# Optimization experiments

Hardware: AMD Instinct MI355X
Metric: run time of the kernel (lower is better)

## Reference

```python
import jax, jax.numpy as jnp
import numpy as np

EMBED = 384
N_HEADS = 6
HEAD_SIZE = EMBED // N_HEADS
B, T = 4, 2048
EPS = 1e-5


def _layernorm(x, g, b):
    mu = jnp.mean(x, axis=-1, keepdims=True)
    var = jnp.mean(jnp.square(x - mu), axis=-1, keepdims=True)
    return (x - mu) * jax.lax.rsqrt(var + EPS) * g + b


def setup_inputs() -> dict:
    key = jax.random.key(0)
    ks = jax.random.split(key, 6)
    s = 0.02
    return {
        "x": jax.random.normal(ks[0], (B, T, EMBED), jnp.float32),
        "Wq": jax.random.normal(ks[1], (N_HEADS, HEAD_SIZE, EMBED), jnp.float32) * s,
        "Wo": jax.random.normal(ks[2], (EMBED, EMBED), jnp.float32) * s,
        "bo": jnp.zeros((EMBED,), jnp.float32),
        "W1": jax.random.normal(ks[3], (EMBED, EMBED), jnp.float32) * s,
        "b1": jnp.zeros((EMBED,), jnp.float32),
        "W2": jax.random.normal(ks[4], (EMBED, EMBED), jnp.float32) * s,
        "b2": jnp.zeros((EMBED,), jnp.float32),
        "g1": jnp.ones((EMBED,), jnp.float32),
        "be1": jnp.zeros((EMBED,), jnp.float32),
        "g2": jnp.ones((EMBED,), jnp.float32),
        "be2": jnp.zeros((EMBED,), jnp.float32),
    }


def reference(x, Wq, Wo, bo, W1, b1, W2, b2, g1, be1, g2, be2):
    # NOTE: original Head uses self.query for q, k AND v (a bug we reproduce):
    # q = k = v = x @ Wq^T per head.
    q = jnp.einsum("bte,hde->bhtd", x, Wq)  # [B,H,T,D]
    scale = HEAD_SIZE ** -0.5
    scores = jnp.einsum("bhtd,bhsd->bhts", q, q) * scale  # [B,H,T,T]
    # torch.tril zeros the upper triangle, then masked_fill(tmp==0, -inf)
    tril = jnp.tril(jnp.ones((T, T), bool))
    scores = jnp.where(tril, scores, 0.0)
    scores = jnp.where(scores == 0.0, -jnp.inf, scores)
    attn = jax.nn.softmax(scores, axis=-1)
    head_out = jnp.einsum("bhts,bhsd->bhtd", attn, q)  # [B,H,T,D]
    cat = head_out.transpose(0, 2, 1, 3).reshape(B, T, EMBED)  # concat heads
    sa = cat @ Wo.T + bo
    x = _layernorm(x + sa, g1, be1)
    ff = jax.nn.relu(x @ W1.T + b1) @ W2.T + b2
    return _layernorm(x + ff, g2, be2)
```

## Files before the change

### kernel.cpp

```cpp
#include <hip/hip_runtime.h>
#include <math.h>

#define BB 4
#define TT 2048
#define EE 384
#define HH 6
#define DD 64
#define MM (BB*TT)

typedef __attribute__((ext_vector_type(8))) short bf16x8;
typedef __attribute__((ext_vector_type(4))) float f32x4;

__device__ __forceinline__ unsigned short f2bf(float f) {
    unsigned int u = __float_as_uint(f);
    u = (u + 0x7FFFu + ((u >> 16) & 1u)) >> 16;
    return (unsigned short)u;
}
__device__ __forceinline__ float bf2f(unsigned short u) {
    return __uint_as_float(((unsigned int)u) << 16);
}
__device__ __forceinline__ unsigned int pk2(float a, float b) {
    return (unsigned int)f2bf(a) | ((unsigned int)f2bf(b) << 16);
}
__device__ __forceinline__ unsigned int cvtpk(float lo, float hi) {
    unsigned int r;
    asm("v_cvt_pk_bf16_f32 %0, %1, %2" : "=v"(r) : "v"(lo), "v"(hi));
    return r;
}

__global__ __launch_bounds__(256) void k_cvt(const float* __restrict__ wq,
                                             const float* __restrict__ wo,
                                             const float* __restrict__ w1,
                                             const float* __restrict__ w2,
                                             unsigned short* __restrict__ wqb,
                                             unsigned short* __restrict__ wob,
                                             unsigned short* __restrict__ w1b,
                                             unsigned short* __restrict__ w2b)
{
    int wi = blockIdx.x / 144, off = (blockIdx.x % 144) * 256;
    const float* s4[4] = {wq, wo, w1, w2};
    unsigned short* d4[4] = {wqb, wob, w1b, w2b};
    const float* src = s4[wi]; unsigned short* dst = d4[wi];
    int i = off + threadIdx.x;
    float4 v = ((const float4*)src)[i];
    uint2 o; o.x = pk2(v.x, v.y); o.y = pk2(v.z, v.w);
    ((uint2*)dst)[i] = o;
}

__global__ __launch_bounds__(256, 2) void k_qgemm(const float* __restrict__ x,
                                                  const unsigned short* __restrict__ W,
                                                  unsigned short* __restrict__ qbf,
                                                  unsigned short* __restrict__ qbfT)
{
    __shared__ unsigned short Xs[32][396];
    __shared__ unsigned short Ts[32][200];
    const int tid = threadIdx.x;
    const int w = tid >> 6, lane = tid & 63;
    const int fr = lane & 15, quad = lane >> 4;
    const int m0 = blockIdx.x * 32;
    const int n0 = blockIdx.y * 192 + w * 48;
    const unsigned short* Wp = W + (size_t)(n0 + fr) * EE + quad * 8;

    {
        const float* xp = x + (size_t)m0 * EE;
        #pragma unroll
        for (int it = 0; it < 12; it++) {
            int idx = it * 1024 + tid * 4;
            int row = idx / EE, col = idx % EE;
            float4 v = *(const float4*)(xp + idx);
            uint2 o; o.x = pk2(v.x, v.y); o.y = pk2(v.z, v.w);
            *(uint2*)&Xs[row][col] = o;
        }
    }

    f32x4 acc[2][3];
    bf16x8 bC[3], bN[3], bT[3];
    #pragma unroll
    for (int mt = 0; mt < 2; mt++)
        #pragma unroll
        for (int nt = 0; nt < 3; nt++) acc[mt][nt] = (f32x4){0.f, 0.f, 0.f, 0.f};
    #pragma unroll
    for (int nt = 0; nt < 3; nt++) bC[nt] = *(const bf16x8*)(Wp + (size_t)nt * 16 * EE);
    #pragma unroll
    for (int nt = 0; nt < 3; nt++) bN[nt] = *(const bf16x8*)(Wp + (size_t)nt * 16 * EE + 32);
    #pragma unroll
    for (int nt = 0; nt < 3; nt++) bT[nt] = bN[nt];
    __syncthreads();

    #pragma unroll
    for (int k0 = 0; k0 < 12; k0++) {
        if (k0 < 10) {
            #pragma unroll
            for (int nt = 0; nt < 3; nt++)
                bT[nt] = *(const bf16x8*)(Wp + (size_t)nt * 16 * EE + (k0 + 2) * 32);
        }
        bf16x8 a0 = *(const bf16x8*)&Xs[fr][k0 * 32 + quad * 8];
        bf16x8 a1 = *(const bf16x8*)&Xs[16 + fr][k0 * 32 + quad * 8];
        #pragma unroll
        for (int nt = 0; nt < 3; nt++) {
            acc[0][nt] = __builtin_amdgcn_mfma_f32_16x16x32_bf16(a0, bC[nt], acc[0][nt], 0, 0, 0);
            acc[1][nt] = __builtin_amdgcn_mfma_f32_16x16x32_bf16(a1, bC[nt], acc[1][nt], 0, 0, 0);
        }
        #pragma unroll
        for (int nt = 0; nt < 3; nt++) { bC[nt] = bN[nt]; bN[nt] = bT[nt]; }
    }

    const int bglob = m0 >> 11, t0 = m0 & 2047;
    #pragma unroll
    for (int nt = 0; nt < 3; nt++) {
        int nl = w * 48 + nt * 16 + fr;
        int n = blockIdx.y * 192 + nl;
        int h = n >> 6, d = n & 63;
        #pragma unroll
        for (int mt = 0; mt < 2; mt++)
            #pragma unroll
            for (int r = 0; r < 4; r++) {
                int ml = mt * 16 + quad * 4 + r;
                unsigned short bf = f2bf(acc[mt][nt][r]);
                qbf[((size_t)(bglob * HH + h) * TT + t0 + ml) * DD + d] = bf;
                Ts[ml][nl] = bf;
            }
    }
    __syncthreads();
    if (tid < 192) {
        int nl = tid;
        int n = blockIdx.y * 192 + nl;
        int h = n >> 6, d = n & 63;
        unsigned short tmp[32];
        #pragma unroll
        for (int i = 0; i < 32; i++) tmp[i] = Ts[i][nl];
        unsigned short* dst = qbfT + ((size_t)(bglob * HH + h) * DD + d) * TT + t0;
        *(uint4*)(dst)      = *(const uint4*)&tmp[0];
        *(uint4*)(dst + 8)  = *(const uint4*)&tmp[8];
        *(uint4*)(dst + 16) = *(const uint4*)&tmp[16];
        *(uint4*)(dst + 24) = *(const uint4*)&tmp[24];
    }
}

__global__ __launch_bounds__(256, 4) void k_attn(const unsigned short* __restrict__ qbf,
                                                 const unsigned short* __restrict__ qbfT,
                                                 unsigned short* __restrict__ cat)
{
    __shared__ unsigned short Ks[2][64][72];
    __shared__ unsigned short Vs[2][64][72];
    __shared__ unsigned short Ps[32][72];
    __shared__ float lsc[32];
    float (*Oc)[68] = (float(*)[68])&Ks[0][0][0];

    const int id = blockIdx.x;
    const int xcd = id & 7, j = id >> 3;
    const int bh = xcd * 3 + (j % 3);
    const int p = j / 3;
    const int bb = bh / HH, hh = bh % HH;
    const int tid = threadIdx.x;
    const int w = tid >> 6, lane = tid & 63;
    const int qhalf = w & 1, keyhalf = w >> 1;
    const int fr = lane & 15, quad = lane >> 4;
    const int fc = quad * 8;
    const unsigned short* qb  = qbf  + (size_t)bh * TT * DD;
    const unsigned short* qtb = qbfT + (size_t)bh * DD * TT;
    const int lr = tid >> 2, lc = (tid & 3) * 16;
    const float EXSC = 0.18033688011112042f;

    #pragma unroll 1
    for (int ph = 0; ph < 2; ph++) {
        const int tile = ph ? (63 - p) : p;
        const int m0 = tile * 32;
        const int nkt = (tile >> 1) + 1;

        uint4 kr0, kr1, vr0, vr1;
        {
            const unsigned short* kp = qb + (size_t)lr * DD + lc;
            kr0 = *(const uint4*)(kp);
            kr1 = *(const uint4*)(kp + 8);
            const unsigned short* vp = qtb + (size_t)lr * TT + lc;
            vr0 = *(const uint4*)(vp);
            vr1 = *(const uint4*)(vp + 8);
        }
        const unsigned short* qp = qb + (size_t)(m0 + qhalf * 16 + fr) * DD + fc;
        const bf16x8 qA0 = *(const bf16x8*)(qp);
        const bf16x8 qA1 = *(const bf16x8*)(qp + 32);

        __syncthreads();
        *(uint4*)&Ks[0][lr][lc]     = kr0;
        *(uint4*)&Ks[0][lr][lc + 8] = kr1;
        *(uint4*)&Vs[0][lr][lc]     = vr0;
        *(uint4*)&Vs[0][lr][lc + 8] = vr1;
        __syncthreads();

        f32x4 accO[4];
        #pragma unroll
        for (int dt = 0; dt < 4; dt++) accO[dt] = (f32x4){0.f, 0.f, 0.f, 0.f};
        float ls[4] = {0.f, 0.f, 0.f, 0.f};
        const int rowbase = m0 + qhalf * 16 + quad * 4;
        const int prow = qhalf * 16 + quad * 4;

        for (int kt = 0; kt < nkt; kt++) {
            const int cur = kt & 1;
            const int s0 = kt * 64;
            if (kt < nkt - 1) {
                const unsigned short* kp = qb + (size_t)(s0 + 64 + lr) * DD + lc;
                kr0 = *(const uint4*)(kp);
                kr1 = *(const uint4*)(kp + 8);
                const unsigned short* vp = qtb + (size_t)lr * TT + s0 + 64 + lc;
                vr0 = *(const uint4*)(vp);
                vr1 = *(const uint4*)(vp + 8);
            }

            f32x4 S[2];
            #pragma unroll
            for (int nt = 0; nt < 2; nt++) {
                f32x4 acc = (f32x4){0.f, 0.f, 0.f, 0.f};
                bf16x8 b0 = *(const bf16x8*)&Ks[cur][keyhalf * 32 + nt * 16 + fr][fc];
                acc = __builtin_amdgcn_mfma_f32_16x16x32_bf16(qA0, b0, acc, 0, 0, 0);
                bf16x8 b1 = *(const bf16x8*)&Ks[cur][keyhalf * 32 + nt * 16 + fr][fc + 32];
                acc = __builtin_amdgcn_mfma_f32_16x16x32_bf16(qA1, b1, acc, 0, 0, 0);
                S[nt] = acc;
            }

            const bool edge = (kt == nkt - 1);
            #pragma unroll
            for (int nt = 0; nt < 2; nt++) {
                const int col = keyhalf * 32 + nt * 16 + fr;
                float pv[4];
                if (edge) {
                    const int jg = s0 + col;
                    #pragma unroll
                    for (int r = 0; r < 4; r++) {
                        float s = S[nt][r];
                        pv[r] = (jg <= rowbase + r && s != 0.0f)
                                ? __builtin_amdgcn_exp2f(s * EXSC) : 0.0f;
                        ls[r] += pv[r];
                    }
                } else {
                    #pragma unroll
                    for (int r = 0; r < 4; r++) {
                        float s = S[nt][r];
                        pv[r] = (s != 0.0f) ? __builtin_amdgcn_exp2f(s * EXSC) : 0.0f;
                        ls[r] += pv[r];
                    }
                }
                unsigned int pk0 = cvtpk(pv[0], pv[1]);
                unsigned int pk1 = cvtpk(pv[2], pv[3]);
                Ps[prow + 0][col] = (unsigned short)(pk0);
                Ps[prow + 1][col] = (unsigned short)(pk0 >> 16);
                Ps[prow + 2][col] = (unsigned short)(pk1);
                Ps[prow + 3][col] = (unsigned short)(pk1 >> 16);
            }

            bf16x8 pA = *(const bf16x8*)&Ps[qhalf * 16 + fr][keyhalf * 32 + fc];
            #pragma unroll
            for (int dt = 0; dt < 4; dt++) {
                bf16x8 v0 = *(const bf16x8*)&Vs[cur][dt * 16 + fr][keyhalf * 32 + fc];
                accO[dt] = __builtin_amdgcn_mfma_f32_16x16x32_bf16(pA, v0, accO[dt], 0, 0, 0);
            }

            if (kt < nkt - 1) {
                *(uint4*)&Ks[cur ^ 1][lr][lc]     = kr0;
                *(uint4*)&Ks[cur ^ 1][lr][lc + 8] = kr1;
                *(uint4*)&Vs[cur ^ 1][lr][lc]     = vr0;
                *(uint4*)&Vs[cur ^ 1][lr][lc + 8] = vr1;
                __syncthreads();
            }
        }

        __syncthreads();
        #pragma unroll
        for (int r = 0; r < 4; r++) {
            #pragma unroll
            for (int o = 1; o < 16; o <<= 1) ls[r] += __shfl_xor(ls[r], o, 64);
        }
        if (keyhalf == 1) {
            #pragma unroll
            for (int dt = 0; dt < 4; dt++)
                #pragma unroll
                for (int r = 0; r < 4; r++)
                    Oc[prow + r][dt * 16 + fr] = accO[dt][r];
            if (fr == 0) {
                #pragma unroll
                for (int r = 0; r < 4; r++) lsc[prow + r] = ls[r];
            }
        }
        __syncthreads();
        if (keyhalf == 0) {
            float il[4];
            #pragma unroll
            for (int r = 0; r < 4; r++) il[r] = 1.0f / (ls[r] + lsc[prow + r]);
            #pragma unroll
            for (int dt = 0; dt < 4; dt++) {
                #pragma unroll
                for (int r = 0; r < 4; r++) {
                    float o = accO[dt][r] + Oc[prow + r][dt * 16 + fr];
                    int t = rowbase + r;
                    cat[((size_t)bb * TT + t) * EE + hh * DD + dt * 16 + fr] =
                        f2bf(o * il[r]);
                }
            }
        }
    }
}

__global__ __launch_bounds__(512, 2) void k_ffn(const unsigned short* __restrict__ catb,
                                                const unsigned short* __restrict__ wob,
                                                const float* __restrict__ bo,
                                                const float* __restrict__ x,
                                                const float* __restrict__ g1,
                                                const float* __restrict__ be1,
                                                const unsigned short* __restrict__ w1b,
                                                const float* __restrict__ b1,
                                                const unsigned short* __restrict__ w2b,
                                                const float* __restrict__ b2,
                                                const float* __restrict__ g2,
                                                const float* __restrict__ be2,
                                                float* __restrict__ out)
{
    __shared__ unsigned short X1s[32][392];
    __shared__ unsigned short H1s[32][392];
    __shared__ float ssum[32][8];
    __shared__ float ssq[32][8];
    const int tid = threadIdx.x;
    const int w = tid >> 6, lane = tid & 63;
    const int fr = lane & 15, quad = lane >> 4;
    const int m0 = blockIdx.x * 32;
    const int n0 = w * 48;

    f32x4 acc[2][3];
    bf16x8 bC[3], bN[3], bT[3];
    const unsigned short* Wp1 = w1b + (size_t)(n0 + fr) * EE + quad * 8;
    const unsigned short* Wp2 = w2b + (size_t)(n0 + fr) * EE + quad * 8;

    {
        const unsigned short* Ap0 = catb + (size_t)(m0 + fr) * EE + quad * 8;
        const unsigned short* Ap1 = Ap0 + 16 * EE;
        const unsigned short* Wp = wob + (size_t)(n0 + fr) * EE + quad * 8;
        #pragma unroll
        for (int mt = 0; mt < 2; mt++)
            #pragma unroll
            for (int nt = 0; nt < 3; nt++) acc[mt][nt] = (f32x4){0.f, 0.f, 0.f, 0.f};
        #pragma unroll
        for (int nt = 0; nt < 3; nt++) bC[nt] = *(const bf16x8*)(Wp + (size_t)nt * 16 * EE);
        #pragma unroll
        for (int nt = 0; nt < 3; nt++) bN[nt] = *(const bf16x8*)(Wp + (size_t)nt * 16 * EE + 32);
        #pragma unroll
        for (int nt = 0; nt < 3; nt++) bT[nt] = bN[nt];
        bf16x8 aC0 = *(const bf16x8*)(Ap0);
        bf16x8 aC1 = *(const bf16x8*)(Ap1);
        bf16x8 aN0 = *(const bf16x8*)(Ap0 + 32);
        bf16x8 aN1 = *(const bf16x8*)(Ap1 + 32);
        bf16x8 aT0 = aN0, aT1 = aN1;
        #pragma unroll
        for (int k0 = 0; k0 < 12; k0++) {
            if (k0 < 10) {
                #pragma unroll
                for (int nt = 0; nt < 3; nt++)
                    bT[nt] = *(const bf16x8*)(Wp + (size_t)nt * 16 * EE + (k0 + 2) * 32);
                aT0 = *(const bf16x8*)(Ap0 + (k0 + 2) * 32);
                aT1 = *(const bf16x8*)(Ap1 + (k0 + 2) * 32);
            }
            #pragma unroll
            for (int nt = 0; nt < 3; nt++) {
                acc[0][nt] = __builtin_amdgcn_mfma_f32_16x16x32_bf16(aC0, bC[nt], acc[0][nt], 0, 0, 0);
                acc[1][nt] = __builtin_amdgcn_mfma_f32_16x16x32_bf16(aC1, bC[nt], acc[1][nt], 0, 0, 0);
            }
            aC0 = aN0; aC1 = aN1; aN0 = aT0; aN1 = aT1;
            #pragma unroll
            for (int nt = 0; nt < 3; nt++) { bC[nt] = bN[nt]; bN[nt] = bT[nt]; }
        }
    }
    #pragma unroll
    for (int nt = 0; nt < 3; nt++) bC[nt] = *(const bf16x8*)(Wp1 + (size_t)nt * 16 * EE);
    #pragma unroll
    for (int nt = 0; nt < 3; nt++) bN[nt] = *(const bf16x8*)(Wp1 + (size_t)nt * 16 * EE + 32);
    {
        float s1[2][4] = {{0.f,0.f,0.f,0.f},{0.f,0.f,0.f,0.f}};
        float s2[2][4] = {{0.f,0.f,0.f,0.f},{0.f,0.f,0.f,0.f}};
        #pragma unroll
        for (int nt = 0; nt < 3; nt++) {
            int n = n0 + nt * 16 + fr;
            float bv = bo[n];
            #pragma unroll
            for (int mt = 0; mt < 2; mt++)
                #pragma unroll
                for (int r = 0; r < 4; r++) {
                    float v = acc[mt][nt][r] + bv
                            + x[(size_t)(m0 + mt * 16 + quad * 4 + r) * EE + n];
                    acc[mt][nt][r] = v;
                    s1[mt][r] += v;
                    s2[mt][r] += v * v;
                }
        }
        #pragma unroll
        for (int mt = 0; mt < 2; mt++)
            #pragma unroll
            for (int r = 0; r < 4; r++) {
                #pragma unroll
                for (int o = 1; o < 16; o <<= 1) {
                    s1[mt][r] += __shfl_xor(s1[mt][r], o, 64);
                    s2[mt][r] += __shfl_xor(s2[mt][r], o, 64);
                }
            }
        if (fr == 0) {
            #pragma unroll
            for (int mt = 0; mt < 2; mt++)
                #pragma unroll
                for (int r = 0; r < 4; r++) {
                    ssum[mt * 16 + quad * 4 + r][w] = s1[mt][r];
                    ssq [mt * 16 + quad * 4 + r][w] = s2[mt][r];
                }
        }
    }
    __syncthreads();
    {
        #pragma unroll
        for (int mt = 0; mt < 2; mt++) {
            float mu[4], rs[4];
            #pragma unroll
            for (int r = 0; r < 4; r++) {
                int row = mt * 16 + quad * 4 + r;
                float t1 = 0.f, t2 = 0.f;
                #pragma unroll
                for (int q = 0; q < 8; q++) { t1 += ssum[row][q]; t2 += ssq[row][q]; }
                mu[r] = t1 * (1.0f / EE);
                float var = t2 * (1.0f / EE) - mu[r] * mu[r];
                rs[r] = rsqrtf(var + 1e-5f);
            }
            #pragma unroll
            for (int nt = 0; nt < 3; nt++) {
                int n = n0 + nt * 16 + fr;
                float gv = g1[n], bev = be1[n];
                #pragma unroll
                for (int r = 0; r < 4; r++) {
                    float v = (acc[mt][nt][r] - mu[r]) * rs[r] * gv + bev;
                    X1s[mt * 16 + quad * 4 + r][n] = f2bf(v);
                }
            }
        }
    }
    __syncthreads();

    {
        #pragma unroll
        for (int mt = 0; mt < 2; mt++)
            #pragma unroll
            for (int nt = 0; nt < 3; nt++) acc[mt][nt] = (f32x4){0.f, 0.f, 0.f, 0.f};
        #pragma unroll
        for (int nt = 0; nt < 3; nt++) bT[nt] = bN[nt];
        #pragma unroll
        for (int k0 = 0; k0 < 12; k0++) {
            if (k0 < 10) {
                #pragma unroll
                for (int nt = 0; nt < 3; nt++)
                    bT[nt] = *(const bf16x8*)(Wp1 + (size_t)nt * 16 * EE + (k0 + 2) * 32);
            }
            bf16x8 a0 = *(const bf16x8*)&X1s[fr][k0 * 32 + quad * 8];
            bf16x8 a1 = *(const bf16x8*)&X1s[16 + fr][k0 * 32 + quad * 8];
            #pragma unroll
            for (int nt = 0; nt < 3; nt++) {
                acc[0][nt] = __builtin_amdgcn_mfma_f32_16x16x32_bf16(a0, bC[nt], acc[0][nt], 0, 0, 0);
                acc[1][nt] = __builtin_amdgcn_mfma_f32_16x16x32_bf16(a1, bC[nt], acc[1][nt], 0, 0, 0);
            }
            #pragma unroll
            for (int nt = 0; nt < 3; nt++) { bC[nt] = bN[nt]; bN[nt] = bT[nt]; }
        }
        #pragma unroll
        for (int nt = 0; nt < 3; nt++) bC[nt] = *(const bf16x8*)(Wp2 + (size_t)nt * 16 * EE);
        #pragma unroll
        for (int nt = 0; nt < 3; nt++) bN[nt] = *(const bf16x8*)(Wp2 + (size_t)nt * 16 * EE + 32);
        #pragma unroll
        for (int nt = 0; nt < 3; nt++) {
            int n = n0 + nt * 16 + fr;
            float bv = b1[n];
            #pragma unroll
            for (int mt = 0; mt < 2; mt++)
                #pragma unroll
                for (int r = 0; r < 4; r++)
                    H1s[mt * 16 + quad * 4 + r][n] = f2bf(fmaxf(acc[mt][nt][r] + bv, 0.0f));
        }
    }
    __syncthreads();

    {
        #pragma unroll
        for (int mt = 0; mt < 2; mt++)
            #pragma unroll
            for (int nt = 0; nt < 3; nt++) acc[mt][nt] = (f32x4){0.f, 0.f, 0.f, 0.f};
        #pragma unroll
        for (int nt = 0; nt < 3; nt++) bT[nt] = bN[nt];
        #pragma unroll
        for (int k0 = 0; k0 < 12; k0++) {
            if (k0 < 10) {
                #pragma unroll
                for (int nt = 0; nt < 3; nt++)
                    bT[nt] = *(const bf16x8*)(Wp2 + (size_t)nt * 16 * EE + (k0 + 2) * 32);
            }
            bf16x8 a0 = *(const bf16x8*)&H1s[fr][k0 * 32 + quad * 8];
            bf16x8 a1 = *(const bf16x8*)&H1s[16 + fr][k0 * 32 + quad * 8];
            #pragma unroll
            for (int nt = 0; nt < 3; nt++) {
                acc[0][nt] = __builtin_amdgcn_mfma_f32_16x16x32_bf16(a0, bC[nt], acc[0][nt], 0, 0, 0);
                acc[1][nt] = __builtin_amdgcn_mfma_f32_16x16x32_bf16(a1, bC[nt], acc[1][nt], 0, 0, 0);
            }
            #pragma unroll
            for (int nt = 0; nt < 3; nt++) { bC[nt] = bN[nt]; bN[nt] = bT[nt]; }
        }
    }
    {
        float s1[2][4] = {{0.f,0.f,0.f,0.f},{0.f,0.f,0.f,0.f}};
        float s2[2][4] = {{0.f,0.f,0.f,0.f},{0.f,0.f,0.f,0.f}};
        #pragma unroll
        for (int nt = 0; nt < 3; nt++) {
            int n = n0 + nt * 16 + fr;
            float bv = b2[n];
            #pragma unroll
            for (int mt = 0; mt < 2; mt++)
                #pragma unroll
                for (int r = 0; r < 4; r++) {
                    float v = acc[mt][nt][r] + bv + bf2f(X1s[mt * 16 + quad * 4 + r][n]);
                    acc[mt][nt][r] = v;
                    s1[mt][r] += v;
                    s2[mt][r] += v * v;
                }
        }
        #pragma unroll
        for (int mt = 0; mt < 2; mt++)
            #pragma unroll
            for (int r = 0; r < 4; r++) {
                #pragma unroll
                for (int o = 1; o < 16; o <<= 1) {
                    s1[mt][r] += __shfl_xor(s1[mt][r], o, 64);
                    s2[mt][r] += __shfl_xor(s2[mt][r], o, 64);
                }
            }
        if (fr == 0) {
            #pragma unroll
            for (int mt = 0; mt < 2; mt++)
                #pragma unroll
                for (int r = 0; r < 4; r++) {
                    ssum[mt * 16 + quad * 4 + r][w] = s1[mt][r];
                    ssq [mt * 16 + quad * 4 + r][w] = s2[mt][r];
                }
        }
    }
    __syncthreads();
    {
        #pragma unroll
        for (int mt = 0; mt < 2; mt++) {
            float mu[4], rs[4];
            #pragma unroll
            for (int r = 0; r < 4; r++) {
                int row = mt * 16 + quad * 4 + r;
                float u1 = 0.f, u2 = 0.f;
                #pragma unroll
                for (int q = 0; q < 8; q++) { u1 += ssum[row][q]; u2 += ssq[row][q]; }
                mu[r] = u1 * (1.0f / EE);
                float var = u2 * (1.0f / EE) - mu[r] * mu[r];
                rs[r] = rsqrtf(var + 1e-5f);
            }
            #pragma unroll
            for (int nt = 0; nt < 3; nt++) {
                int n = n0 + nt * 16 + fr;
                float gv = g2[n], bev = be2[n];
                #pragma unroll
                for (int r = 0; r < 4; r++)
                    out[(size_t)(m0 + mt * 16 + quad * 4 + r) * EE + n] =
                        (acc[mt][nt][r] - mu[r]) * rs[r] * gv + bev;
            }
        }
    }
}

extern "C" void kernel_launch(void* const* d_in, const int* in_sizes, int n_in,
                              void* d_out, int out_size, void* d_ws, size_t ws_size,
                              hipStream_t stream) {
    (void)in_sizes; (void)n_in; (void)out_size; (void)ws_size;
    const float* x   = (const float*)d_in[0];
    const float* Wq  = (const float*)d_in[1];
    const float* Wo  = (const float*)d_in[2];
    const float* bo  = (const float*)d_in[3];
    const float* W1  = (const float*)d_in[4];
    const float* b1  = (const float*)d_in[5];
    const float* W2  = (const float*)d_in[6];
    const float* b2  = (const float*)d_in[7];
    const float* g1  = (const float*)d_in[8];
    const float* be1 = (const float*)d_in[9];
    const float* g2  = (const float*)d_in[10];
    const float* be2 = (const float*)d_in[11];
    float* out = (float*)d_out;

    float* ws = (float*)d_ws;
    const size_t SZ = (size_t)MM * EE;
    float* S1 = ws + SZ;
    float* S2 = ws + 2 * SZ;
    float* S3 = ws + 3 * SZ;

    unsigned short* qbf  = (unsigned short*)S1;
    unsigned short* qbfT = qbf + (size_t)BB * HH * TT * DD;
    unsigned short* catb = (unsigned short*)S2;
    unsigned short* wqb  = (unsigned short*)S3;
    unsigned short* wob  = wqb + (size_t)EE * EE;
    unsigned short* w1b  = wob + (size_t)EE * EE;
    unsigned short* w2b  = w1b + (size_t)EE * EE;

    k_cvt<<<dim3(4 * 144), dim3(256), 0, stream>>>(Wq, Wo, W1, W2, wqb, wob, w1b, w2b);
    k_qgemm<<<dim3(MM / 32, 2), dim3(256), 0, stream>>>(x, wqb, qbf, qbfT);
    k_attn<<<dim3(768), dim3(256), 0, stream>>>(qbf, qbfT, catb);
    k_ffn<<<dim3(MM / 32), dim3(512), 0, stream>>>(catb, wob, bo, x, g1, be1,
                                                   w1b, b1, w2b, b2, g2, be2, out);
}
```

Baseline: 174.2 us.

## Process both causal query tiles concurrently in one 512-thread block sharing K/V

The attention kernel now runs its paired query tiles (p and 63-p) at the same time in two 256-thread groups of a 512-thread block, instead of one after the other. Each K/V tile is loaded from global memory into shared memory once and used by both groups. This removes the duplicated K/V traffic and the second prologue and epilogue. In exchange, the shorter tile's group idles on its later iterations, and the larger block with launch bounds (512, 6) changes occupancy and register limits.

```diff
diff --git a/kernel.cpp b/kernel.cpp
--- a/kernel.cpp
+++ b/kernel.cpp
@@ -137,14 +137,14 @@
     }
 }
 
-__global__ __launch_bounds__(256, 4) void k_attn(const unsigned short* __restrict__ qbf,
+__global__ __launch_bounds__(512, 6) void k_attn(const unsigned short* __restrict__ qbf,
                                                  const unsigned short* __restrict__ qbfT,
                                                  unsigned short* __restrict__ cat)
 {
     __shared__ unsigned short Ks[2][64][72];
     __shared__ unsigned short Vs[2][64][72];
-    __shared__ unsigned short Ps[32][72];
-    __shared__ float lsc[32];
+    __shared__ unsigned short Ps[64][72];
+    __shared__ float lsc[64];
     float (*Oc)[68] = (float(*)[68])&Ks[0][0][0];
 
     const int id = blockIdx.x;
@@ -154,59 +154,48 @@
     const int bb = bh / HH, hh = bh % HH;
     const int tid = threadIdx.x;
     const int w = tid >> 6, lane = tid & 63;
-    const int qhalf = w & 1, keyhalf = w >> 1;
+    const int tg = w >> 2, wv = w & 3;
+    const int qhalf = wv & 1, keyhalf = wv >> 1;
     const int fr = lane & 15, quad = lane >> 4;
     const int fc = quad * 8;
     const unsigned short* qb  = qbf  + (size_t)bh * TT * DD;
     const unsigned short* qtb = qbfT + (size_t)bh * DD * TT;
-    const int lr = tid >> 2, lc = (tid & 3) * 16;
+    const int lr = tid >> 3, lc = (tid & 7) * 8;
     const float EXSC = 0.18033688011112042f;
 
-    #pragma unroll 1
-    for (int ph = 0; ph < 2; ph++) {
-        const int tile = ph ? (63 - p) : p;
-        const int m0 = tile * 32;
-        const int nkt = (tile >> 1) + 1;
-
-        uint4 kr0, kr1, vr0, vr1;
-        {
-            const unsigned short* kp = qb + (size_t)lr * DD + lc;
-            kr0 = *(const uint4*)(kp);
-            kr1 = *(const uint4*)(kp + 8);
-            const unsigned short* vp = qtb + (size_t)lr * TT + lc;
-            vr0 = *(const uint4*)(vp);
-            vr1 = *(const uint4*)(vp + 8);
-        }
-        const unsigned short* qp = qb + (size_t)(m0 + qhalf * 16 + fr) * DD + fc;
-        const bf16x8 qA0 = *(const bf16x8*)(qp);
-        const bf16x8 qA1 = *(const bf16x8*)(qp + 32);
-
-        __syncthreads();
-        *(uint4*)&Ks[0][lr][lc]     = kr0;
-        *(uint4*)&Ks[0][lr][lc + 8] = kr1;
-        *(uint4*)&Vs[0][lr][lc]     = vr0;
-        *(uint4*)&Vs[0][lr][lc + 8] = vr1;
-        __syncthreads();
-
-        f32x4 accO[4];
-        #pragma unroll
-        for (int dt = 0; dt < 4; dt++) accO[dt] = (f32x4){0.f, 0.f, 0.f, 0.f};
-        float ls[4] = {0.f, 0.f, 0.f, 0.f};
-        const int rowbase = m0 + qhalf * 16 + quad * 4;
-        const int prow = qhalf * 16 + quad * 4;
-
-        for (int kt = 0; kt < nkt; kt++) {
-            const int cur = kt & 1;
-            const int s0 = kt * 64;
-            if (kt < nkt - 1) {
-                const unsigned short* kp = qb + (size_t)(s0 + 64 + lr) * DD + lc;
-                kr0 = *(const uint4*)(kp);
-                kr1 = *(const uint4*)(kp + 8);
-                const unsigned short* vp = qtb + (size_t)lr * TT + s0 + 64 + lc;
-                vr0 = *(const uint4*)(vp);
-                vr1 = *(const uint4*)(vp + 8);
-            }
-
+    const int tile = tg ? (63 - p) : p;
+    const int m0 = tile * 32;
+    const int nkt = (tile >> 1) + 1;
+    const int nktB = ((63 - p) >> 1) + 1;
+
+    {
+        uint4 kr = *(const uint4*)(qb + (size_t)lr * DD + lc);
+        uint4 vr = *(const uint4*)(qtb + (size_t)lr * TT + lc);
+        *(uint4*)&Ks[0][lr][lc] = kr;
+        *(uint4*)&Vs[0][lr][lc] = vr;
+    }
+    const unsigned short* qp = qb + (size_t)(m0 + qhalf * 16 + fr) * DD + fc;
+    const bf16x8 qA0 = *(const bf16x8*)(qp);
+    const bf16x8 qA1 = *(const bf16x8*)(qp + 32);
+    __syncthreads();
+
+    f32x4 accO[4];
+    #pragma unroll
+    for (int dt = 0; dt < 4; dt++) accO[dt] = (f32x4){0.f, 0.f, 0.f, 0.f};
+    float ls[4] = {0.f, 0.f, 0.f, 0.f};
+    const int rowbase = m0 + qhalf * 16 + quad * 4;
+    const int prow = tg * 32 + qhalf * 16 + quad * 4;
+
+    uint4 kr, vr;
+    for (int kt = 0; kt < nktB; kt++) {
+        const int cur = kt & 1;
+        const int s0 = kt * 64;
+        if (kt < nktB - 1) {
+            kr = *(const uint4*)(qb + (size_t)(s0 + 64 + lr) * DD + lc);
+            vr = *(const uint4*)(qtb + (size_t)lr * TT + s0 + 64 + lc);
+        }
+
+        if (kt < nkt) {
             f32x4 S[2];
             #pragma unroll
             for (int nt = 0; nt < 2; nt++) {
@@ -248,53 +237,51 @@
                 Ps[prow + 3][col] = (unsigned short)(pk1 >> 16);
             }
 
-            bf16x8 pA = *(const bf16x8*)&Ps[qhalf * 16 + fr][keyhalf * 32 + fc];
+            bf16x8 pA = *(const bf16x8*)&Ps[tg * 32 + qhalf * 16 + fr][keyhalf * 32 + fc];
             #pragma unroll
             for (int dt = 0; dt < 4; dt++) {
                 bf16x8 v0 = *(const bf16x8*)&Vs[cur][dt * 16 + fr][keyhalf * 32 + fc];
                 accO[dt] = __builtin_amdgcn_mfma_f32_16x16x32_bf16(pA, v0, accO[dt], 0, 0, 0);
             }
-
-            if (kt < nkt - 1) {
-                *(uint4*)&Ks[cur ^ 1][lr][lc]     = kr0;
-                *(uint4*)&Ks[cur ^ 1][lr][lc + 8] = kr1;
-                *(uint4*)&Vs[cur ^ 1][lr][lc]     = vr0;
-                *(uint4*)&Vs[cur ^ 1][lr][lc + 8] = vr1;
-                __syncthreads();
-            }
-        }
-
-        __syncthreads();
-        #pragma unroll
-        for (int r = 0; r < 4; r++) {
-            #pragma unroll
-            for (int o = 1; o < 16; o <<= 1) ls[r] += __shfl_xor(ls[r], o, 64);
-        }
-        if (keyhalf == 1) {
-            #pragma unroll
-            for (int dt = 0; dt < 4; dt++)
-                #pragma unroll
-                for (int r = 0; r < 4; r++)
-                    Oc[prow + r][dt * 16 + fr] = accO[dt][r];
-            if (fr == 0) {
-                #pragma unroll
-                for (int r = 0; r < 4; r++) lsc[prow + r] = ls[r];
-            }
-        }
-        __syncthreads();
-        if (keyhalf == 0) {
-            float il[4];
-            #pragma unroll
-            for (int r = 0; r < 4; r++) il[r] = 1.0f / (ls[r] + lsc[prow + r]);
-            #pragma unroll
-            for (int dt = 0; dt < 4; dt++) {
-                #pragma unroll
-                for (int r = 0; r < 4; r++) {
-                    float o = accO[dt][r] + Oc[prow + r][dt * 16 + fr];
-                    int t = rowbase + r;
-                    cat[((size_t)bb * TT + t) * EE + hh * DD + dt * 16 + fr] =
-                        f2bf(o * il[r]);
-                }
+        }
+
+        if (kt < nktB - 1) {
+            *(uint4*)&Ks[cur ^ 1][lr][lc] = kr;
+            *(uint4*)&Vs[cur ^ 1][lr][lc] = vr;
+            __syncthreads();
+        }
+    }
+
+    __syncthreads();
+    #pragma unroll
+    for (int r = 0; r < 4; r++) {
+        #pragma unroll
+        for (int o = 1; o < 16; o <<= 1) ls[r] += __shfl_xor(ls[r], o, 64);
+    }
+    if (keyhalf == 1) {
+        #pragma unroll
+        for (int dt = 0; dt < 4; dt++)
+            #pragma unroll
+            for (int r = 0; r < 4; r++)
+                Oc[prow + r][dt * 16 + fr] = accO[dt][r];
+        if (fr == 0) {
+            #pragma unroll
+            for (int r = 0; r < 4; r++) lsc[prow + r] = ls[r];
+        }
+    }
+    __syncthreads();
+    if (keyhalf == 0) {
+        float il[4];
+        #pragma unroll
+        for (int r = 0; r < 4; r++) il[r] = 1.0f / (ls[r] + lsc[prow + r]);
+        #pragma unroll
+        for (int dt = 0; dt < 4; dt++) {
+            #pragma unroll
+            for (int r = 0; r < 4; r++) {
+                float o = accO[dt][r] + Oc[prow + r][dt * 16 + fr];
+                int t = rowbase + r;
+                cat[((size_t)bb * TT + t) * EE + hh * DD + dt * 16 + fr] =
+                    f2bf(o * il[r]);
             }
         }
     }
@@ -603,7 +590,7 @@
 
     k_cvt<<<dim3(4 * 144), dim3(256), 0, stream>>>(Wq, Wo, W1, W2, wqb, wob, w1b, w2b);
     k_qgemm<<<dim3(MM / 32, 2), dim3(256), 0, stream>>>(x, wqb, qbf, qbfT);
-    k_attn<<<dim3(768), dim3(256), 0, stream>>>(qbf, qbfT, catb);
+    k_attn<<<dim3(768), dim3(512), 0, stream>>>(qbf, qbfT, catb);
     k_ffn<<<dim3(MM / 32), dim3(512), 0, stream>>>(catb, wob, bo, x, g1, be1,
                                                    w1b, b1, w2b, b2, g2, be2, out);
 }
```

After: 168.7 us. 3.2% less time.
